# Optimization experiments

Hardware: AMD Instinct MI355X
Metric: run time of the kernel (lower is better)

Reference implementation:

```python
import jax, jax.numpy as jnp
import numpy as np

O, I, B = 4096, 4096, 4096  # out_features, in_features, flattened tokens
GROUP = 128
INIT_PEAK = 2.0


def setup_inputs() -> dict:
    key = jax.random.key(0)
    k1, k2, k3, k4 = jax.random.split(key, 4)
    x = jax.random.normal(k1, (B, I), jnp.float32)
    # initial_ternary in {-1,0,1} -> theta init per the torch constructor
    tern = jax.random.randint(k2, (O, I), -1, 2)
    theta_neg = jnp.where(tern == -1, INIT_PEAK, -INIT_PEAK).astype(jnp.float32)
    theta_pos = jnp.where(tern == 1, INIT_PEAK, -INIT_PEAK).astype(jnp.float32)
    # per-group scales expanded to full weight shape (scales.unsqueeze(1).expand.reshape)
    n_groups = O * I // GROUP
    scales = jax.random.uniform(k3, (n_groups,), jnp.float32, 0.01, 0.05)
    scales_exp = jnp.repeat(scales, GROUP).reshape(O, I)
    # reparameterization noise (training path), made explicit for determinism
    eps = jax.random.normal(k4, (B, O), jnp.float32)
    return {"x": x, "theta_neg": theta_neg, "theta_pos": theta_pos,
            "scales_exp": scales_exp, "eps": eps}


def reference(x, theta_neg, theta_pos, scales_exp, eps):
    # stable 3-way softmax over logits [theta_neg, 0, theta_pos], done without
    # materializing the stacked [O, I, 3] tensor
    m = jnp.maximum(jnp.maximum(theta_neg, theta_pos), 0.0)
    e_neg = jnp.exp(theta_neg - m)
    e_zero = jnp.exp(-m)
    e_pos = jnp.exp(theta_pos - m)
    Z = e_neg + e_zero + e_pos
    p_neg = e_neg / Z
    p_pos = e_pos / Z
    diff = p_pos - p_neg
    w_mean = diff * scales_exp                                   # [O, I]
    w_var = (p_pos + p_neg - diff * diff) * (scales_exp * scales_exp)  # [O, I]
    mu = x @ w_mean.T                                            # [B, O]
    sigma_sq = (x * x) @ w_var.T                                 # [B, O]
    sigma = jnp.sqrt(jnp.maximum(sigma_sq, 1e-8))
    return mu + sigma * eps
```

## Files before the change

### kernel.cpp

```cpp
#include <hip/hip_runtime.h>

#define I_DIM 4096
#define O_DIM 4096
#define B_DIM 4096

typedef __bf16 bf16;
typedef __attribute__((ext_vector_type(8))) __bf16 bf16x8;
typedef __attribute__((ext_vector_type(4))) float f32x4;

__device__ inline unsigned short f2bf_bits(float f) {
    unsigned u = __builtin_bit_cast(unsigned, f);
    unsigned r = 0x7fffu + ((u >> 16) & 1u);
    return (unsigned short)((u + r) >> 16);
}

__global__ void prep_x(const float4* __restrict__ x,
                       ushort4* __restrict__ xb,
                       ushort4* __restrict__ x2b) {
    size_t i = (size_t)blockIdx.x * blockDim.x + threadIdx.x;
    float4 v = x[i];
    ushort4 o1, o2;
    o1.x = f2bf_bits(v.x); o1.y = f2bf_bits(v.y);
    o1.z = f2bf_bits(v.z); o1.w = f2bf_bits(v.w);
    o2.x = f2bf_bits(v.x * v.x); o2.y = f2bf_bits(v.y * v.y);
    o2.z = f2bf_bits(v.z * v.z); o2.w = f2bf_bits(v.w * v.w);
    xb[i] = o1;
    x2b[i] = o2;
}

__device__ inline void lr_wmv(float tn, float tp, float s,
                              unsigned short& wm, unsigned short& wv) {
    float m = fmaxf(fmaxf(tn, tp), 0.0f);
    float en = __expf(tn - m);
    float ez = __expf(-m);
    float ep = __expf(tp - m);
    float inv = 1.0f / (en + ez + ep);
    float pn = en * inv, pp = ep * inv;
    float d = pp - pn;
    wm = f2bf_bits(d * s);
    wv = f2bf_bits((pp + pn - d * d) * (s * s));
}

__global__ void prep_weights(const float4* __restrict__ tn,
                             const float4* __restrict__ tp,
                             const float4* __restrict__ sc,
                             ushort4* __restrict__ wm,
                             ushort4* __restrict__ wv) {
    size_t i = (size_t)blockIdx.x * blockDim.x + threadIdx.x;
    float4 a = tn[i];
    float4 b = tp[i];
    float4 s = sc[i];
    ushort4 om, ov;
    lr_wmv(a.x, b.x, s.x, om.x, ov.x);
    lr_wmv(a.y, b.y, s.y, om.y, ov.y);
    lr_wmv(a.z, b.z, s.z, om.z, ov.z);
    lr_wmv(a.w, b.w, s.w, om.w, ov.w);
    wm[i] = om;
    wv[i] = ov;
}

#define BM 128
#define BN 128
#define BK 32

__device__ inline void gl_lds16(const bf16* g, bf16* l) {
    __builtin_amdgcn_global_load_lds(
        (const __attribute__((address_space(1))) unsigned int*)g,
        (__attribute__((address_space(3))) unsigned int*)l,
        16, 0, 0);
}

__global__ __launch_bounds__(256, 2)
void fused_dual_gemm(const bf16* __restrict__ Xb, const bf16* __restrict__ X2b,
                     const bf16* __restrict__ Wm, const bf16* __restrict__ Wv,
                     const float* __restrict__ eps, float* __restrict__ out) {
    __shared__ bf16 sX[BM * BK];
    __shared__ bf16 sX2[BM * BK];
    __shared__ bf16 sWm[BN * BK];
    __shared__ bf16 sWv[BN * BK];

    const int tid  = threadIdx.x;
    const int lane = tid & 63;
    const int wave = tid >> 6;

    const int bm = blockIdx.y * BM;
    const int bn = blockIdx.x * BN;

    const int e0 = wave * 512 + lane * 8;
    const int e1 = e0 + 2048;
    const int r0 = e0 >> 5, c0 = e0 & 31;
    const int r1 = e1 >> 5, c1 = e1 & 31;

    const bf16* gX0  = Xb  + (size_t)(bm + r0) * I_DIM + c0;
    const bf16* gX1  = Xb  + (size_t)(bm + r1) * I_DIM + c1;
    const bf16* gX20 = X2b + (size_t)(bm + r0) * I_DIM + c0;
    const bf16* gX21 = X2b + (size_t)(bm + r1) * I_DIM + c1;
    const bf16* gWm0 = Wm  + (size_t)(bn + r0) * I_DIM + c0;
    const bf16* gWm1 = Wm  + (size_t)(bn + r1) * I_DIM + c1;
    const bf16* gWv0 = Wv  + (size_t)(bn + r0) * I_DIM + c0;
    const bf16* gWv1 = Wv  + (size_t)(bn + r1) * I_DIM + c1;

    bf16* lX0  = sX  + wave * 512;
    bf16* lX1  = sX  + wave * 512 + 2048;
    bf16* lX20 = sX2 + wave * 512;
    bf16* lX21 = sX2 + wave * 512 + 2048;
    bf16* lWm0 = sWm + wave * 512;
    bf16* lWm1 = sWm + wave * 512 + 2048;
    bf16* lWv0 = sWv + wave * 512;
    bf16* lWv1 = sWv + wave * 512 + 2048;

    const int fr = lane & 15;
    const int fk = (lane >> 4) << 3;
    const int m0 = (wave >> 1) << 6;
    const int n0 = (wave & 1) << 6;

    f32x4 accM[4][4];
    f32x4 accV[4][4];
    const f32x4 z = {0.0f, 0.0f, 0.0f, 0.0f};
#pragma unroll
    for (int mi = 0; mi < 4; ++mi)
#pragma unroll
        for (int ni = 0; ni < 4; ++ni) { accM[mi][ni] = z; accV[mi][ni] = z; }

    for (int k0 = 0; k0 < I_DIM; k0 += BK) {
        __syncthreads();
        gl_lds16(gX0  + k0, lX0);
        gl_lds16(gX1  + k0, lX1);
        gl_lds16(gX20 + k0, lX20);
        gl_lds16(gX21 + k0, lX21);
        gl_lds16(gWm0 + k0, lWm0);
        gl_lds16(gWm1 + k0, lWm1);
        gl_lds16(gWv0 + k0, lWv0);
        gl_lds16(gWv1 + k0, lWv1);
        __syncthreads();

        bf16x8 ax[4], ax2[4];
#pragma unroll
        for (int mi = 0; mi < 4; ++mi) {
            const int row = m0 + mi * 16 + fr;
            ax[mi]  = *(const bf16x8*)&sX [row * BK + fk];
            ax2[mi] = *(const bf16x8*)&sX2[row * BK + fk];
        }
#pragma unroll
        for (int ni = 0; ni < 4; ++ni) {
            const int rowb = n0 + ni * 16 + fr;
            bf16x8 bm_ = *(const bf16x8*)&sWm[rowb * BK + fk];
            bf16x8 bv_ = *(const bf16x8*)&sWv[rowb * BK + fk];
#pragma unroll
            for (int mi = 0; mi < 4; ++mi) {
                accM[mi][ni] = __builtin_amdgcn_mfma_f32_16x16x32_bf16(
                    ax[mi], bm_, accM[mi][ni], 0, 0, 0);
                accV[mi][ni] = __builtin_amdgcn_mfma_f32_16x16x32_bf16(
                    ax2[mi], bv_, accV[mi][ni], 0, 0, 0);
            }
        }
    }

    const int oc = lane & 15;
    const int orb = (lane >> 4) << 2;
#pragma unroll
    for (int mi = 0; mi < 4; ++mi) {
#pragma unroll
        for (int ni = 0; ni < 4; ++ni) {
            const int gn = bn + n0 + ni * 16 + oc;
            const int gm = bm + m0 + mi * 16 + orb;
#pragma unroll
            for (int r = 0; r < 4; ++r) {
                const size_t off = (size_t)(gm + r) * O_DIM + gn;
                const float mu = accM[mi][ni][r];
                const float vv = accV[mi][ni][r];
                out[off] = fmaf(sqrtf(fmaxf(vv, 1e-8f)), eps[off], mu);
            }
        }
    }
}

extern "C" void kernel_launch(void* const* d_in, const int* in_sizes, int n_in,
                              void* d_out, int out_size, void* d_ws, size_t ws_size,
                              hipStream_t stream) {
    const float* x   = (const float*)d_in[0];
    const float* tn  = (const float*)d_in[1];
    const float* tp  = (const float*)d_in[2];
    const float* sc  = (const float*)d_in[3];
    const float* eps = (const float*)d_in[4];
    float* out = (float*)d_out;

    const size_t NE = (size_t)O_DIM * I_DIM;
    unsigned short* xb  = (unsigned short*)d_ws;
    unsigned short* x2b = xb + NE;
    unsigned short* wm  = x2b + NE;
    unsigned short* wv  = wm + NE;

    const int pblocks = (int)(NE / 4 / 256);
    prep_x<<<pblocks, 256, 0, stream>>>((const float4*)x, (ushort4*)xb, (ushort4*)x2b);
    prep_weights<<<pblocks, 256, 0, stream>>>((const float4*)tn, (const float4*)tp,
                                              (const float4*)sc, (ushort4*)wm, (ushort4*)wv);

    dim3 grid(O_DIM / BN, B_DIM / BM);
    fused_dual_gemm<<<grid, 256, 0, stream>>>(
        (const bf16*)xb, (const bf16*)x2b, (const bf16*)wm, (const bf16*)wv, eps, out);
}
```

Before: 640.2 us.

## Double GEMM K-tile with XOR-swizzled LDS layout and merge prep kernels

Raises the GEMM K tile from 32 to 64 so each pair of barriers covers twice as many MFMAs. It also adds an XOR swizzle on the LDS column groups to avoid bank conflicts on the fragment reads. The two elementwise prep kernels become one launch, with wider 16-byte stores for x and a hardware reciprocal in place of a divide. LDS use per block doubles to 64KB, which may limit residency of the two blocks per CU requested by the launch bounds.

```diff
diff --git a/kernel.cpp b/kernel.cpp
--- a/kernel.cpp
+++ b/kernel.cpp
@@ -7,25 +7,12 @@
 typedef __bf16 bf16;
 typedef __attribute__((ext_vector_type(8))) __bf16 bf16x8;
 typedef __attribute__((ext_vector_type(4))) float f32x4;
+typedef __attribute__((ext_vector_type(8))) unsigned short ushort8;
 
 __device__ inline unsigned short f2bf_bits(float f) {
     unsigned u = __builtin_bit_cast(unsigned, f);
     unsigned r = 0x7fffu + ((u >> 16) & 1u);
     return (unsigned short)((u + r) >> 16);
-}
-
-__global__ void prep_x(const float4* __restrict__ x,
-                       ushort4* __restrict__ xb,
-                       ushort4* __restrict__ x2b) {
-    size_t i = (size_t)blockIdx.x * blockDim.x + threadIdx.x;
-    float4 v = x[i];
-    ushort4 o1, o2;
-    o1.x = f2bf_bits(v.x); o1.y = f2bf_bits(v.y);
-    o1.z = f2bf_bits(v.z); o1.w = f2bf_bits(v.w);
-    o2.x = f2bf_bits(v.x * v.x); o2.y = f2bf_bits(v.y * v.y);
-    o2.z = f2bf_bits(v.z * v.z); o2.w = f2bf_bits(v.w * v.w);
-    xb[i] = o1;
-    x2b[i] = o2;
 }
 
 __device__ inline void lr_wmv(float tn, float tp, float s,
@@ -34,34 +21,53 @@
     float en = __expf(tn - m);
     float ez = __expf(-m);
     float ep = __expf(tp - m);
-    float inv = 1.0f / (en + ez + ep);
+    float inv = __builtin_amdgcn_rcpf(en + ez + ep);
     float pn = en * inv, pp = ep * inv;
     float d = pp - pn;
     wm = f2bf_bits(d * s);
     wv = f2bf_bits((pp + pn - d * d) * (s * s));
 }
 
-__global__ void prep_weights(const float4* __restrict__ tn,
-                             const float4* __restrict__ tp,
-                             const float4* __restrict__ sc,
-                             ushort4* __restrict__ wm,
-                             ushort4* __restrict__ wv) {
-    size_t i = (size_t)blockIdx.x * blockDim.x + threadIdx.x;
-    float4 a = tn[i];
-    float4 b = tp[i];
-    float4 s = sc[i];
-    ushort4 om, ov;
-    lr_wmv(a.x, b.x, s.x, om.x, ov.x);
-    lr_wmv(a.y, b.y, s.y, om.y, ov.y);
-    lr_wmv(a.z, b.z, s.z, om.z, ov.z);
-    lr_wmv(a.w, b.w, s.w, om.w, ov.w);
-    wm[i] = om;
-    wv[i] = ov;
+__global__ void prep_all(const float4* __restrict__ x,
+                         ushort8* __restrict__ xb8, ushort8* __restrict__ x2b8,
+                         const float4* __restrict__ tn, const float4* __restrict__ tp,
+                         const float4* __restrict__ sc,
+                         ushort4* __restrict__ wm, ushort4* __restrict__ wv,
+                         int nbx) {
+    const int bid = blockIdx.x;
+    if (bid < nbx) {
+        size_t i = (size_t)bid * blockDim.x + threadIdx.x;
+        float4 a = x[2 * i];
+        float4 b = x[2 * i + 1];
+        ushort8 o1, o2;
+        o1[0] = f2bf_bits(a.x); o1[1] = f2bf_bits(a.y);
+        o1[2] = f2bf_bits(a.z); o1[3] = f2bf_bits(a.w);
+        o1[4] = f2bf_bits(b.x); o1[5] = f2bf_bits(b.y);
+        o1[6] = f2bf_bits(b.z); o1[7] = f2bf_bits(b.w);
+        o2[0] = f2bf_bits(a.x * a.x); o2[1] = f2bf_bits(a.y * a.y);
+        o2[2] = f2bf_bits(a.z * a.z); o2[3] = f2bf_bits(a.w * a.w);
+        o2[4] = f2bf_bits(b.x * b.x); o2[5] = f2bf_bits(b.y * b.y);
+        o2[6] = f2bf_bits(b.z * b.z); o2[7] = f2bf_bits(b.w * b.w);
+        xb8[i] = o1;
+        x2b8[i] = o2;
+    } else {
+        size_t i = (size_t)(bid - nbx) * blockDim.x + threadIdx.x;
+        float4 a = tn[i];
+        float4 b = tp[i];
+        float4 s = sc[i];
+        ushort4 om, ov;
+        lr_wmv(a.x, b.x, s.x, om.x, ov.x);
+        lr_wmv(a.y, b.y, s.y, om.y, ov.y);
+        lr_wmv(a.z, b.z, s.z, om.z, ov.z);
+        lr_wmv(a.w, b.w, s.w, om.w, ov.w);
+        wm[i] = om;
+        wv[i] = ov;
+    }
 }
 
 #define BM 128
 #define BN 128
-#define BK 32
+#define BK 64
 
 __device__ inline void gl_lds16(const bf16* g, bf16* l) {
     __builtin_amdgcn_global_load_lds(
@@ -86,31 +92,26 @@
     const int bm = blockIdx.y * BM;
     const int bn = blockIdx.x * BN;
 
-    const int e0 = wave * 512 + lane * 8;
-    const int e1 = e0 + 2048;
-    const int r0 = e0 >> 5, c0 = e0 & 31;
-    const int r1 = e1 >> 5, c1 = e1 & 31;
-
-    const bf16* gX0  = Xb  + (size_t)(bm + r0) * I_DIM + c0;
-    const bf16* gX1  = Xb  + (size_t)(bm + r1) * I_DIM + c1;
-    const bf16* gX20 = X2b + (size_t)(bm + r0) * I_DIM + c0;
-    const bf16* gX21 = X2b + (size_t)(bm + r1) * I_DIM + c1;
-    const bf16* gWm0 = Wm  + (size_t)(bn + r0) * I_DIM + c0;
-    const bf16* gWm1 = Wm  + (size_t)(bn + r1) * I_DIM + c1;
-    const bf16* gWv0 = Wv  + (size_t)(bn + r0) * I_DIM + c0;
-    const bf16* gWv1 = Wv  + (size_t)(bn + r1) * I_DIM + c1;
-
-    bf16* lX0  = sX  + wave * 512;
-    bf16* lX1  = sX  + wave * 512 + 2048;
-    bf16* lX20 = sX2 + wave * 512;
-    bf16* lX21 = sX2 + wave * 512 + 2048;
-    bf16* lWm0 = sWm + wave * 512;
-    bf16* lWm1 = sWm + wave * 512 + 2048;
-    bf16* lWv0 = sWv + wave * 512;
-    bf16* lWv1 = sWv + wave * 512 + 2048;
-
-    const int fr = lane & 15;
-    const int fk = (lane >> 4) << 3;
+    const int rowoff = lane >> 3;
+    const int cgoff  = ((lane & 7) ^ rowoff) << 3;
+
+    const bf16* gX[4]; const bf16* gX2[4]; const bf16* gWm[4]; const bf16* gWv[4];
+    int ldsoff[4];
+#pragma unroll
+    for (int j = 0; j < 4; ++j) {
+        const int c = wave + 4 * j;
+        const size_t ra = (size_t)(bm + c * 8 + rowoff) * I_DIM + cgoff;
+        const size_t rb = (size_t)(bn + c * 8 + rowoff) * I_DIM + cgoff;
+        gX[j]  = Xb  + ra;
+        gX2[j] = X2b + ra;
+        gWm[j] = Wm  + rb;
+        gWv[j] = Wv  + rb;
+        ldsoff[j] = c << 9;
+    }
+
+    const int fr  = lane & 15;
+    const int cg0 = lane >> 4;
+    const int sw0 = (cg0 ^ (fr & 7)) << 3;
     const int m0 = (wave >> 1) << 6;
     const int n0 = (wave & 1) << 6;
 
@@ -124,39 +125,42 @@
 
     for (int k0 = 0; k0 < I_DIM; k0 += BK) {
         __syncthreads();
-        gl_lds16(gX0  + k0, lX0);
-        gl_lds16(gX1  + k0, lX1);
-        gl_lds16(gX20 + k0, lX20);
-        gl_lds16(gX21 + k0, lX21);
-        gl_lds16(gWm0 + k0, lWm0);
-        gl_lds16(gWm1 + k0, lWm1);
-        gl_lds16(gWv0 + k0, lWv0);
-        gl_lds16(gWv1 + k0, lWv1);
+#pragma unroll
+        for (int j = 0; j < 4; ++j) {
+            gl_lds16(gX[j]  + k0, sX  + ldsoff[j]);
+            gl_lds16(gX2[j] + k0, sX2 + ldsoff[j]);
+            gl_lds16(gWm[j] + k0, sWm + ldsoff[j]);
+            gl_lds16(gWv[j] + k0, sWv + ldsoff[j]);
+        }
         __syncthreads();
 
-        bf16x8 ax[4], ax2[4];
-#pragma unroll
-        for (int mi = 0; mi < 4; ++mi) {
-            const int row = m0 + mi * 16 + fr;
-            ax[mi]  = *(const bf16x8*)&sX [row * BK + fk];
-            ax2[mi] = *(const bf16x8*)&sX2[row * BK + fk];
-        }
-#pragma unroll
-        for (int ni = 0; ni < 4; ++ni) {
-            const int rowb = n0 + ni * 16 + fr;
-            bf16x8 bm_ = *(const bf16x8*)&sWm[rowb * BK + fk];
-            bf16x8 bv_ = *(const bf16x8*)&sWv[rowb * BK + fk];
+#pragma unroll
+        for (int kh = 0; kh < 2; ++kh) {
+            const int sw = sw0 ^ (kh << 5);
+            bf16x8 ax[4], ax2[4];
 #pragma unroll
             for (int mi = 0; mi < 4; ++mi) {
-                accM[mi][ni] = __builtin_amdgcn_mfma_f32_16x16x32_bf16(
-                    ax[mi], bm_, accM[mi][ni], 0, 0, 0);
-                accV[mi][ni] = __builtin_amdgcn_mfma_f32_16x16x32_bf16(
-                    ax2[mi], bv_, accV[mi][ni], 0, 0, 0);
+                const int row = m0 + mi * 16 + fr;
+                ax[mi]  = *(const bf16x8*)&sX [row * BK + sw];
+                ax2[mi] = *(const bf16x8*)&sX2[row * BK + sw];
+            }
+#pragma unroll
+            for (int ni = 0; ni < 4; ++ni) {
+                const int rowb = n0 + ni * 16 + fr;
+                bf16x8 bm_ = *(const bf16x8*)&sWm[rowb * BK + sw];
+                bf16x8 bv_ = *(const bf16x8*)&sWv[rowb * BK + sw];
+#pragma unroll
+                for (int mi = 0; mi < 4; ++mi) {
+                    accM[mi][ni] = __builtin_amdgcn_mfma_f32_16x16x32_bf16(
+                        ax[mi], bm_, accM[mi][ni], 0, 0, 0);
+                    accV[mi][ni] = __builtin_amdgcn_mfma_f32_16x16x32_bf16(
+                        ax2[mi], bv_, accV[mi][ni], 0, 0, 0);
+                }
             }
         }
     }
 
-    const int oc = lane & 15;
+    const int oc  = lane & 15;
     const int orb = (lane >> 4) << 2;
 #pragma unroll
     for (int mi = 0; mi < 4; ++mi) {
@@ -191,10 +195,12 @@
     unsigned short* wm  = x2b + NE;
     unsigned short* wv  = wm + NE;
 
-    const int pblocks = (int)(NE / 4 / 256);
-    prep_x<<<pblocks, 256, 0, stream>>>((const float4*)x, (ushort4*)xb, (ushort4*)x2b);
-    prep_weights<<<pblocks, 256, 0, stream>>>((const float4*)tn, (const float4*)tp,
-                                              (const float4*)sc, (ushort4*)wm, (ushort4*)wv);
+    const int nbx = (int)(NE / 8 / 256);
+    const int nbw = (int)(NE / 4 / 256);
+    prep_all<<<nbx + nbw, 256, 0, stream>>>(
+        (const float4*)x, (ushort8*)xb, (ushort8*)x2b,
+        (const float4*)tn, (const float4*)tp, (const float4*)sc,
+        (ushort4*)wm, (ushort4*)wv, nbx);
 
     dim3 grid(O_DIM / BN, B_DIM / BM);
     fused_dual_gemm<<<grid, 256, 0, stream>>>(
```

Result: faster. 610.9 us (-4.6%).
